# Optimization experiments

Measured on AMD Instinct MI355X. Metric: run time of the kernel, lower is better.

The kernel has to match this reference:

```python
import math
import jax, jax.numpy as jnp
import numpy as np

B, Q, K, N, F = 4096, 1024, 256, 16384, 512


def setup_inputs() -> dict:
    key = jax.random.key(0)
    ks = jax.random.split(key, 6)
    return {
        "pooled_h": jax.random.normal(ks[0], (B, Q), jnp.float32),
        "snapshot_keys": jax.random.normal(ks[1], (N, K), jnp.float32),
        "snapshot_embs": jax.random.normal(ks[2], (N, F), jnp.float32),
        "Wq": jax.random.normal(ks[3], (Q, K), jnp.float32) / math.sqrt(Q),
        "bq": jnp.zeros((K,), jnp.float32),
        "Wb": jax.random.normal(ks[4], (Q, 1), jnp.float32) / math.sqrt(Q),
        "bb": jnp.zeros((1,), jnp.float32),
        "fallback": jnp.zeros((F,), jnp.float32),
        "topk": 2,
    }


def reference(pooled_h, snapshot_keys, snapshot_embs, Wq, bq, Wb, bb, fallback, topk):
    # q = q_proj(pooled_h)                                  [B, K]
    q = pooled_h @ Wq + bq
    # scores = q @ keys^T / sqrt(key_dim)                   [B, N]
    scores = (q @ snapshot_keys.T) / jnp.sqrt(jnp.asarray(q.shape[-1], q.dtype))
    # top-k values/indices per row, scatter into -inf mask, masked softmax
    vals, idx = jax.lax.top_k(scores, topk)                 # [B, k], [B, k]
    rows = jnp.arange(scores.shape[0])[:, None]             # [B, 1]
    mask = jnp.full_like(scores, -jnp.inf).at[rows, idx].set(vals)
    alpha = jax.nn.softmax(mask, axis=-1)                   # [B, N], k nonzeros/row
    emb_mix = alpha @ snapshot_embs                         # [B, F]
    beta = jax.nn.sigmoid(pooled_h @ Wb + bb)               # [B, 1]
    return emb_mix * beta, alpha
```

## Files before the change

kernel.cpp:

```cpp
#include <hip/hip_runtime.h>
#include <math.h>

#define B_ 4096
#define Q_ 1024
#define KD 256
#define N_ 16384
#define F_ 512

typedef __attribute__((ext_vector_type(8))) short bhalf8;
typedef __attribute__((ext_vector_type(4))) float f32x4;
typedef __attribute__((ext_vector_type(16))) float f32x16;

static __device__ __forceinline__ unsigned short f2bf(float f) {
  unsigned int u = __builtin_bit_cast(unsigned int, f);
  unsigned int r = (u + 0x7fffu + ((u >> 16) & 1u)) >> 16;
  return (unsigned short)r;
}
static __device__ __forceinline__ float bf2f(unsigned short h) {
  return __builtin_bit_cast(float, (unsigned int)h << 16);
}
static __device__ __forceinline__ unsigned umaxu(unsigned a, unsigned b) { return a > b ? a : b; }
static __device__ __forceinline__ unsigned uminu(unsigned a, unsigned b) { return a < b ? a : b; }

__global__ __launch_bounds__(256)
void k_prep(const float* __restrict__ Wq, unsigned short* __restrict__ wqT_hi,
            unsigned short* __restrict__ wqT_lo) {
  __shared__ float tile[64][65];
  const int tid = threadIdx.x;
  const int b = blockIdx.x;
  const int k0 = (b >> 2) * 64, c0 = (b & 3) * 64;
  {
    const int kk = tid >> 2;
    const int cg = (tid & 3) * 16;
#pragma unroll
    for (int i = 0; i < 4; ++i) {
      const float4 x =
          *reinterpret_cast<const float4*>(&Wq[(size_t)(k0 + kk) * KD + c0 + cg + i * 4]);
      tile[kk][cg + i * 4 + 0] = x.x; tile[kk][cg + i * 4 + 1] = x.y;
      tile[kk][cg + i * 4 + 2] = x.z; tile[kk][cg + i * 4 + 3] = x.w;
    }
  }
  __syncthreads();
  {
    const int cc = tid >> 2;
    const int kg = (tid & 3) * 16;
    bhalf8 h0, h1, l0, l1;
#pragma unroll
    for (int i = 0; i < 16; ++i) {
      const float v = tile[kg + i][cc];
      const unsigned short h = f2bf(v);
      const unsigned short l = f2bf(v - bf2f(h));
      if (i < 8) { h0[i] = (short)h; l0[i] = (short)l; }
      else       { h1[i - 8] = (short)h; l1[i - 8] = (short)l; }
    }
    const size_t o = (size_t)(c0 + cc) * Q_ + k0 + kg;
    *reinterpret_cast<bhalf8*>(&wqT_hi[o]) = h0;
    *reinterpret_cast<bhalf8*>(&wqT_hi[o + 8]) = h1;
    *reinterpret_cast<bhalf8*>(&wqT_lo[o]) = l0;
    *reinterpret_cast<bhalf8*>(&wqT_lo[o + 8]) = l1;
  }
}

__global__ __launch_bounds__(256)
void k_qproj_mfma(const float* __restrict__ ph,
                  const unsigned short* __restrict__ wqT_hi,
                  const unsigned short* __restrict__ wqT_lo,
                  const float* __restrict__ bq, float* __restrict__ q,
                  unsigned short* __restrict__ qbf,
                  const float* __restrict__ keys,
                  unsigned short* __restrict__ kbf) {
  __shared__ float red[4][32][64];
  const int tid = threadIdx.x;
  const int bid = blockIdx.x;

  if (bid >= 512) {
    const size_t base = ((size_t)(bid - 512) * 256 + tid) * 8;
    const float4 x = *reinterpret_cast<const float4*>(&keys[base]);
    const float4 y = *reinterpret_cast<const float4*>(&keys[base + 4]);
    bhalf8 o;
    o[0] = (short)f2bf(x.x); o[1] = (short)f2bf(x.y);
    o[2] = (short)f2bf(x.z); o[3] = (short)f2bf(x.w);
    o[4] = (short)f2bf(y.x); o[5] = (short)f2bf(y.y);
    o[6] = (short)f2bf(y.z); o[7] = (short)f2bf(y.w);
    *reinterpret_cast<bhalf8*>(&kbf[base]) = o;
    return;
  }

  const int wave = tid >> 6, lane = tid & 63;
  const int l31 = lane & 31, lhi = lane >> 5;
  const int c0 = (bid & 3) * 64;
  const int r0 = (bid >> 2) * 32;
  const int k0 = wave * 256;

  const float* pa = ph + (size_t)(r0 + l31) * Q_ + k0 + lhi * 8;
  const unsigned short* pb0_h = wqT_hi + (size_t)(c0 + l31) * Q_ + k0 + lhi * 8;
  const unsigned short* pb0_l = wqT_lo + (size_t)(c0 + l31) * Q_ + k0 + lhi * 8;
  const unsigned short* pb1_h = wqT_hi + (size_t)(c0 + 32 + l31) * Q_ + k0 + lhi * 8;
  const unsigned short* pb1_l = wqT_lo + (size_t)(c0 + 32 + l31) * Q_ + k0 + lhi * 8;

  f32x16 acc0 = {}, acc1 = {};
#pragma unroll
  for (int s = 0; s < 16; ++s) {
    const int ko = s * 16;
    const float4 va = *reinterpret_cast<const float4*>(pa + ko);
    const float4 vb = *reinterpret_cast<const float4*>(pa + ko + 4);
    float v[8];
    v[0] = va.x; v[1] = va.y; v[2] = va.z; v[3] = va.w;
    v[4] = vb.x; v[5] = vb.y; v[6] = vb.z; v[7] = vb.w;
    bhalf8 ah, al;
#pragma unroll
    for (int j = 0; j < 8; ++j) {
      const unsigned short h = f2bf(v[j]);
      ah[j] = (short)h;
      al[j] = (short)f2bf(v[j] - bf2f(h));
    }
    const bhalf8 b0h = *reinterpret_cast<const bhalf8*>(pb0_h + ko);
    const bhalf8 b0l = *reinterpret_cast<const bhalf8*>(pb0_l + ko);
    const bhalf8 b1h = *reinterpret_cast<const bhalf8*>(pb1_h + ko);
    const bhalf8 b1l = *reinterpret_cast<const bhalf8*>(pb1_l + ko);
    acc0 = __builtin_amdgcn_mfma_f32_32x32x16_bf16(ah, b0h, acc0, 0, 0, 0);
    acc0 = __builtin_amdgcn_mfma_f32_32x32x16_bf16(ah, b0l, acc0, 0, 0, 0);
    acc0 = __builtin_amdgcn_mfma_f32_32x32x16_bf16(al, b0h, acc0, 0, 0, 0);
    acc1 = __builtin_amdgcn_mfma_f32_32x32x16_bf16(ah, b1h, acc1, 0, 0, 0);
    acc1 = __builtin_amdgcn_mfma_f32_32x32x16_bf16(ah, b1l, acc1, 0, 0, 0);
    acc1 = __builtin_amdgcn_mfma_f32_32x32x16_bf16(al, b1h, acc1, 0, 0, 0);
  }

#pragma unroll
  for (int r = 0; r < 16; ++r) {
    const int rl = (r & 3) + 8 * (r >> 2) + 4 * lhi;
    red[wave][rl][l31] = acc0[r];
    red[wave][rl][32 + l31] = acc1[r];
  }
  __syncthreads();
  {
    const int rr = tid >> 3, cb = (tid & 7) * 8;
    float s[8] = {};
#pragma unroll
    for (int w = 0; w < 4; ++w) {
      const float4 t0 = *reinterpret_cast<const float4*>(&red[w][rr][cb]);
      const float4 t1 = *reinterpret_cast<const float4*>(&red[w][rr][cb + 4]);
      s[0] += t0.x; s[1] += t0.y; s[2] += t0.z; s[3] += t0.w;
      s[4] += t1.x; s[5] += t1.y; s[6] += t1.z; s[7] += t1.w;
    }
    const float4 b0 = *reinterpret_cast<const float4*>(&bq[c0 + cb]);
    const float4 b1 = *reinterpret_cast<const float4*>(&bq[c0 + cb + 4]);
    s[0] += b0.x; s[1] += b0.y; s[2] += b0.z; s[3] += b0.w;
    s[4] += b1.x; s[5] += b1.y; s[6] += b1.z; s[7] += b1.w;
    const size_t o = (size_t)(r0 + rr) * KD + c0 + cb;
    float4 o0, o1;
    o0.x = s[0]; o0.y = s[1]; o0.z = s[2]; o0.w = s[3];
    o1.x = s[4]; o1.y = s[5]; o1.z = s[6]; o1.w = s[7];
    *reinterpret_cast<float4*>(&q[o]) = o0;
    *reinterpret_cast<float4*>(&q[o + 4]) = o1;
    bhalf8 bv;
#pragma unroll
    for (int j = 0; j < 8; ++j) bv[j] = (short)f2bf(s[j]);
    *reinterpret_cast<bhalf8*>(&qbf[o]) = bv;
  }
}

__global__ __launch_bounds__(256, 4)
void k_scores_mfma(const unsigned short* __restrict__ qbf,
                   const unsigned short* __restrict__ kbf,
                   unsigned* __restrict__ candP, float* __restrict__ outAlpha) {
  __shared__ __align__(16) char lds[32768];
  __shared__ unsigned mbuf[64 * 8];
  const int tid = threadIdx.x;
  const int wave = tid >> 6, lane = tid & 63;
  const int l31 = lane & 31, lhi = lane >> 5;
  const int rh = wave >> 1, ch = wave & 1;
  const int bc = blockIdx.x, br = blockIdx.y;
  const int row0 = br * 64;
  const int m_row = row0 + rh * 32 + l31;

  float4* zb = reinterpret_cast<float4*>(
      (char*)outAlpha + (size_t)(br * 16 + bc) * 262144);
  const float4 z4 = {0.f, 0.f, 0.f, 0.f};

  bhalf8 qf[16];
#pragma unroll
  for (int kt = 0; kt < 16; ++kt)
    qf[kt] = *reinterpret_cast<const bhalf8*>(&qbf[(size_t)m_row * KD + kt * 16 + lhi * 8]);

  auto stage = [&](int bi, int u) {
    const int t = u >> 1, kh = u & 1;
#pragma unroll
    for (int i = 0; i < 4; ++i) {
      const int D = i * 4096 + tid * 16;
      const int colt = D >> 8;
      const int kb = D & 255;
      const int kbs = kb ^ ((colt & 15) << 4);
      const char* src = (const char*)kbf +
          ((size_t)(bc * 1024 + t * 64 + colt) * 512 + kh * 256 + kbs);
      __builtin_amdgcn_global_load_lds(
          (const __attribute__((address_space(1))) unsigned int*)src,
          (__attribute__((address_space(3))) unsigned int*)(lds + bi * 16384 + D),
          16, 0, 0);
    }
  };

  unsigned P1 = 0u, P2 = 0u;
  const int acol = ch * 32 + l31;
  const int swz = (acol & 15) << 4;
  const int kofs = lhi * 16;

  stage(0, 0);
  __syncthreads();

  int buf = 0;
  for (int t = 0; t < 16; ++t) {
    f32x16 acc = {};
#pragma unroll
    for (int kh = 0; kh < 2; ++kh) {
      const int u = t * 2 + kh;
      if (u < 31) stage(buf ^ 1, u + 1);
      zb[u * 512 + tid] = z4;
      zb[u * 512 + 256 + tid] = z4;
      const char* kb = lds + buf * 16384 + acol * 256;
#pragma unroll
      for (int kt = 0; kt < 8; ++kt) {
        const bhalf8 af = *reinterpret_cast<const bhalf8*>(kb + ((kt * 32 + kofs) ^ swz));
        acc = __builtin_amdgcn_mfma_f32_32x32x16_bf16(af, qf[kh * 8 + kt], acc, 0, 0, 0);
      }
      if (kh == 1) {
        const int cb = t * 64 + ch * 32 + lhi * 4;
#pragma unroll
        for (int r = 0; r < 16; ++r) {
          const int rofs = (r & 3) + 8 * (r >> 2);
          const unsigned p =
              (__builtin_bit_cast(unsigned, acc[r] + 512.f) & 0xFFFFF800u) |
              (unsigned)(cb + rofs);
          const unsigned w1 = uminu(P1, p);
          P1 = umaxu(P1, p);
          P2 = umaxu(P2, w1);
        }
      }
      __syncthreads();
      buf ^= 1;
    }
  }

  {
    const int mrow = rh * 32 + l31;
    const int slot = ch * 2 + lhi;
    mbuf[mrow * 8 + slot * 2 + 0] = P1;
    mbuf[mrow * 8 + slot * 2 + 1] = P2;
  }
  __syncthreads();
  if (tid < 64) {
    unsigned T1 = 0u, T2 = 0u, T3 = 0u, T4 = 0u;
#pragma unroll
    for (int j = 0; j < 8; ++j) {
      const unsigned p = mbuf[tid * 8 + j];
      const unsigned w1 = uminu(T1, p); T1 = umaxu(T1, p);
      const unsigned w2 = uminu(T2, w1); T2 = umaxu(T2, w1);
      const unsigned w3 = uminu(T3, w2); T3 = umaxu(T3, w2);
      T4 = umaxu(T4, w3);
    }
    const size_t o = (size_t)(row0 + tid) * 64 + bc * 4;
    candP[o + 0] = T1; candP[o + 1] = T2; candP[o + 2] = T3; candP[o + 3] = T4;
  }
}

__global__ __launch_bounds__(256)
void k_finalize(const float* __restrict__ q, const float* __restrict__ keys,
                const float* __restrict__ ph, const float* __restrict__ Wb,
                const float* __restrict__ bb, const float* __restrict__ embs,
                const unsigned* __restrict__ candP,
                float* __restrict__ outEmb, float* __restrict__ outAlpha) {
  __shared__ float red[4];
  __shared__ int   topIdx[8];
  __shared__ float resc[8];
  __shared__ float sParam[3];
  __shared__ int   sIdx[2];
  const int tid = threadIdx.x;
  const int wave = tid >> 6, lane = tid & 63;
  const int row = blockIdx.x;
  float* arow = outAlpha + (size_t)row * N_;

  {
    const float4 a = *reinterpret_cast<const float4*>(&ph[(size_t)row * Q_ + tid * 4]);
    const float4 w = *reinterpret_cast<const float4*>(&Wb[tid * 4]);
    float s = a.x * w.x + a.y * w.y + a.z * w.z + a.w * w.w;
#pragma unroll
    for (int m = 32; m >= 1; m >>= 1) s += __shfl_xor(s, m);
    if (lane == 0) red[wave] = s;
  }

  if (wave == 0) {
    unsigned p = candP[(size_t)row * 64 + lane];
    const int mycol = (lane >> 2) * 1024 + (int)(p & 0x7FFu);
#pragma unroll
    for (int it = 0; it < 8; ++it) {
      unsigned mx = p;
#pragma unroll
      for (int m = 32; m >= 1; m >>= 1) {
        const unsigned o = (unsigned)__shfl_xor((int)mx, m);
        mx = mx > o ? mx : o;
      }
      const unsigned long long bal = __ballot(p == mx);
      const int src = __ffsll((unsigned long long)bal) - 1;
      if (lane == src) { topIdx[it] = mycol; p = 0u; }
    }
  }
  __syncthreads();

  {
#pragma unroll
    for (int h = 0; h < 2; ++h) {
      const int cnd = topIdx[wave * 2 + h];
      const float4 qv = *reinterpret_cast<const float4*>(&q[(size_t)row * KD + lane * 4]);
      const float4 kv = *reinterpret_cast<const float4*>(&keys[(size_t)cnd * KD + lane * 4]);
      float s = qv.x * kv.x + qv.y * kv.y + qv.z * kv.z + qv.w * kv.w;
#pragma unroll
      for (int m = 32; m >= 1; m >>= 1) s += __shfl_xor(s, m);
      if (lane == 0) resc[wave * 2 + h] = s * 0.0625f;
    }
  }
  __syncthreads();

  if (tid == 0) {
    float w1 = -INFINITY, w2 = -INFINITY; int j1 = 0x7fffffff, j2 = 0x7fffffff;
#pragma unroll
    for (int c = 0; c < 8; ++c) {
      const float v = resc[c]; const int x = topIdx[c];
      const bool beat1 = (v > w1) || (v == w1 && x < j1);
      const bool beat2 = (v > w2) || (v == w2 && x < j2);
      if (beat1) { w2 = w1; j2 = j1; w1 = v; j1 = x; }
      else if (beat2) { w2 = v; j2 = x; }
    }
    const float t = expf(w2 - w1);
    const float inv = 1.f / (1.f + t);
    const float bsum = red[0] + red[1] + red[2] + red[3] + bb[0];
    sParam[0] = inv; sParam[1] = t * inv;
    sParam[2] = 1.f / (1.f + expf(-bsum));
    sIdx[0] = j1; sIdx[1] = j2;
  }
  __syncthreads();

  const float a1 = sParam[0], a2 = sParam[1], beta = sParam[2];
  const int j1 = sIdx[0], j2 = sIdx[1];
  if (tid == 0) { arow[j1] = a1; arow[j2] = a2; }
  if (tid < 128) {
    const int f = tid * 4;
    const float4 e1 = *reinterpret_cast<const float4*>(&embs[(size_t)j1 * F_ + f]);
    const float4 e2 = *reinterpret_cast<const float4*>(&embs[(size_t)j2 * F_ + f]);
    float4 o;
    o.x = beta * (a1 * e1.x + a2 * e2.x);
    o.y = beta * (a1 * e1.y + a2 * e2.y);
    o.z = beta * (a1 * e1.z + a2 * e2.z);
    o.w = beta * (a1 * e1.w + a2 * e2.w);
    *reinterpret_cast<float4*>(&outEmb[(size_t)row * F_ + f]) = o;
  }
}

extern "C" void kernel_launch(void* const* d_in, const int* in_sizes, int n_in,
                              void* d_out, int out_size, void* d_ws, size_t ws_size,
                              hipStream_t stream) {
  const float* ph   = (const float*)d_in[0];
  const float* keys = (const float*)d_in[1];
  const float* embs = (const float*)d_in[2];
  const float* Wq   = (const float*)d_in[3];
  const float* bq   = (const float*)d_in[4];
  const float* Wb   = (const float*)d_in[5];
  const float* bb   = (const float*)d_in[6];

  float* outEmb   = (float*)d_out;
  float* outAlpha = outEmb + (size_t)B_ * F_;

  float*          q      = (float*)d_ws;
  unsigned short* qbf    = (unsigned short*)(q + (size_t)B_ * KD);
  unsigned short* kbf    = qbf + (size_t)B_ * KD;
  unsigned*       candP  = (unsigned*)(kbf + (size_t)N_ * KD);
  unsigned short* wqT_hi = (unsigned short*)(candP + (size_t)B_ * 64);
  unsigned short* wqT_lo = wqT_hi + (size_t)KD * Q_;

  k_prep<<<64, 256, 0, stream>>>(Wq, wqT_hi, wqT_lo);
  k_qproj_mfma<<<2560, 256, 0, stream>>>(ph, wqT_hi, wqT_lo, bq, q, qbf,
                                         keys, kbf);
  k_scores_mfma<<<dim3(16, 64), 256, 0, stream>>>(qbf, kbf, candP, outAlpha);
  k_finalize<<<B_, 256, 0, stream>>>(q, keys, ph, Wb, bb, embs, candP,
                                     outEmb, outAlpha);
}
```

Baseline: 119.8 us.

## Move beta gate into prep kernel and rebalance alpha zeroing across kernels

```diff
diff --git a/kernel.cpp b/kernel.cpp
--- a/kernel.cpp
+++ b/kernel.cpp
@@ -22,12 +22,33 @@
 static __device__ __forceinline__ unsigned umaxu(unsigned a, unsigned b) { return a > b ? a : b; }
 static __device__ __forceinline__ unsigned uminu(unsigned a, unsigned b) { return a < b ? a : b; }
 
+
 __global__ __launch_bounds__(256)
 void k_prep(const float* __restrict__ Wq, unsigned short* __restrict__ wqT_hi,
-            unsigned short* __restrict__ wqT_lo) {
+            unsigned short* __restrict__ wqT_lo,
+            const float* __restrict__ ph, const float* __restrict__ Wb,
+            const float* __restrict__ bb, float* __restrict__ betaArr) {
   __shared__ float tile[64][65];
   const int tid = threadIdx.x;
-  const int b = blockIdx.x;
+  const int bid = blockIdx.x;
+
+  if (bid >= 64) {
+    const int lane = tid & 63, wave = tid >> 6;
+    const int row = (bid - 64) * 4 + wave;
+    float s = 0.f;
+#pragma unroll
+    for (int i = 0; i < 4; ++i) {
+      const float4 a = *reinterpret_cast<const float4*>(&ph[(size_t)row * Q_ + lane * 4 + i * 256]);
+      const float4 w = *reinterpret_cast<const float4*>(&Wb[lane * 4 + i * 256]);
+      s += a.x * w.x + a.y * w.y + a.z * w.z + a.w * w.w;
+    }
+#pragma unroll
+    for (int m = 32; m >= 1; m >>= 1) s += __shfl_xor(s, m);
+    if (lane == 0) betaArr[row] = 1.f / (1.f + expf(-(s + bb[0])));
+    return;
+  }
+
+  const int b = bid;
   const int k0 = (b >> 2) * 64, c0 = (b & 3) * 64;
   {
     const int kk = tid >> 2;
@@ -174,8 +195,7 @@
   const int row0 = br * 64;
   const int m_row = row0 + rh * 32 + l31;
 
-  float4* zb = reinterpret_cast<float4*>(
-      (char*)outAlpha + (size_t)(br * 16 + bc) * 262144);
+  float4* zb = reinterpret_cast<float4*>(outAlpha) + (size_t)(br * 16 + bc) * 16384;
   const float4 z4 = {0.f, 0.f, 0.f, 0.f};
 
   bhalf8 qf[16];
@@ -215,8 +235,12 @@
     for (int kh = 0; kh < 2; ++kh) {
       const int u = t * 2 + kh;
       if (u < 31) stage(buf ^ 1, u + 1);
-      zb[u * 512 + tid] = z4;
-      zb[u * 512 + 256 + tid] = z4;
+      if (u < 24) {
+        const int rsel = u / 6, csel = u - rsel * 6;
+        float4* z = zb + rsel * 4096 + csel * 512;
+        z[tid] = z4;
+        z[256 + tid] = z4;
+      }
       const char* kb = lds + buf * 16384 + acol * 256;
 #pragma unroll
       for (int kt = 0; kt < 8; ++kt) {
@@ -265,14 +289,12 @@
 
 __global__ __launch_bounds__(256)
 void k_finalize(const float* __restrict__ q, const float* __restrict__ keys,
-                const float* __restrict__ ph, const float* __restrict__ Wb,
-                const float* __restrict__ bb, const float* __restrict__ embs,
+                const float* __restrict__ embs, const float* __restrict__ betaArr,
                 const unsigned* __restrict__ candP,
                 float* __restrict__ outEmb, float* __restrict__ outAlpha) {
-  __shared__ float red[4];
   __shared__ int   topIdx[8];
   __shared__ float resc[8];
-  __shared__ float sParam[3];
+  __shared__ float sParam[2];
   __shared__ int   sIdx[2];
   const int tid = threadIdx.x;
   const int wave = tid >> 6, lane = tid & 63;
@@ -280,12 +302,10 @@
   float* arow = outAlpha + (size_t)row * N_;
 
   {
-    const float4 a = *reinterpret_cast<const float4*>(&ph[(size_t)row * Q_ + tid * 4]);
-    const float4 w = *reinterpret_cast<const float4*>(&Wb[tid * 4]);
-    float s = a.x * w.x + a.y * w.y + a.z * w.z + a.w * w.w;
-#pragma unroll
-    for (int m = 32; m >= 1; m >>= 1) s += __shfl_xor(s, m);
-    if (lane == 0) red[wave] = s;
+    float4* a4 = reinterpret_cast<float4*>(arow);
+    const float4 z4 = {0.f, 0.f, 0.f, 0.f};
+#pragma unroll
+    for (int i = 0; i < 4; ++i) a4[3072 + i * 256 + tid] = z4;
   }
 
   if (wave == 0) {
@@ -332,14 +352,13 @@
     }
     const float t = expf(w2 - w1);
     const float inv = 1.f / (1.f + t);
-    const float bsum = red[0] + red[1] + red[2] + red[3] + bb[0];
     sParam[0] = inv; sParam[1] = t * inv;
-    sParam[2] = 1.f / (1.f + expf(-bsum));
     sIdx[0] = j1; sIdx[1] = j2;
   }
   __syncthreads();
 
-  const float a1 = sParam[0], a2 = sParam[1], beta = sParam[2];
+  const float a1 = sParam[0], a2 = sParam[1];
+  const float beta = betaArr[row];
   const int j1 = sIdx[0], j2 = sIdx[1];
   if (tid == 0) { arow[j1] = a1; arow[j2] = a2; }
   if (tid < 128) {
@@ -369,17 +388,18 @@
   float* outEmb   = (float*)d_out;
   float* outAlpha = outEmb + (size_t)B_ * F_;
 
-  float*          q      = (float*)d_ws;
-  unsigned short* qbf    = (unsigned short*)(q + (size_t)B_ * KD);
-  unsigned short* kbf    = qbf + (size_t)B_ * KD;
-  unsigned*       candP  = (unsigned*)(kbf + (size_t)N_ * KD);
-  unsigned short* wqT_hi = (unsigned short*)(candP + (size_t)B_ * 64);
-  unsigned short* wqT_lo = wqT_hi + (size_t)KD * Q_;
-
-  k_prep<<<64, 256, 0, stream>>>(Wq, wqT_hi, wqT_lo);
+  float*          q       = (float*)d_ws;
+  unsigned short* qbf     = (unsigned short*)(q + (size_t)B_ * KD);
+  unsigned short* kbf     = qbf + (size_t)B_ * KD;
+  unsigned*       candP   = (unsigned*)(kbf + (size_t)N_ * KD);
+  unsigned short* wqT_hi  = (unsigned short*)(candP + (size_t)B_ * 64);
+  unsigned short* wqT_lo  = wqT_hi + (size_t)KD * Q_;
+  float*          betaArr = (float*)(wqT_lo + (size_t)KD * Q_);
+
+  k_prep<<<1088, 256, 0, stream>>>(Wq, wqT_hi, wqT_lo, ph, Wb, bb, betaArr);
   k_qproj_mfma<<<2560, 256, 0, stream>>>(ph, wqT_hi, wqT_lo, bq, q, qbf,
                                          keys, kbf);
   k_scores_mfma<<<dim3(16, 64), 256, 0, stream>>>(qbf, kbf, candP, outAlpha);
-  k_finalize<<<B_, 256, 0, stream>>>(q, keys, ph, Wb, bb, embs, candP,
+  k_finalize<<<B_, 256, 0, stream>>>(q, keys, embs, betaArr, candP,
                                      outEmb, outAlpha);
 }
```

New measurement: 119.5 us. About the same (-0.3%).
